# Optimization experiments

Measured on AMD Instinct MI355X. Metric: run time of the kernel, lower is better.

## Reference

```python
import jax, jax.numpy as jnp
import numpy as np

DIM = 180; HEADS = 6; WS = 16; NUM_TOKENS = 64; RDIM = 10; CAT = 128
KS = 5; MLP_HID = 360; DTD = 64; Hh = 64; Ww = 64; B = 8; M = 64


def _ln(x, g, b, eps=1e-5):
    mu = x.mean(-1, keepdims=True)
    var = ((x - mu) ** 2).mean(-1, keepdims=True)
    return (x - mu) / jnp.sqrt(var + eps) * g + b


def _l2norm(x):
    return x / jnp.clip(jnp.linalg.norm(x, axis=-1, keepdims=True), 1e-12)


def setup_inputs() -> dict:
    key = jax.random.key(0)
    ks = jax.random.split(key, 24)
    rn = lambda k, s: jax.random.normal(k, s, jnp.float32) * 0.02
    z = lambda *s: jnp.zeros(s, jnp.float32)
    return {
        'x': jax.random.normal(ks[0], (B, Hh * Ww, DIM), jnp.float32),
        'td': jax.random.normal(ks[1], (B, M, DIM), jnp.float32),
        'norm1_g': jnp.ones((DIM,), jnp.float32), 'norm1_b': z(DIM),
        'wqkv_w': rn(ks[2], (DIM, 3 * DIM)), 'wqkv_b': z(3 * DIM),
        'atd_wq_w': rn(ks[3], (DIM, RDIM)), 'atd_wq_b': z(RDIM),
        'atd_wk_w': rn(ks[4], (DIM, RDIM)), 'atd_wk_b': z(RDIM),
        'atd_wv_w': rn(ks[5], (DIM, DIM)), 'atd_wv_b': z(DIM),
        'atd_scale': jnp.ones((1,), jnp.float32),
        'aca_proj_w': rn(ks[6], (DIM, DIM)), 'aca_proj_b': z(DIM),
        'win_rpb': rn(ks[7], ((2 * WS - 1) ** 2, HEADS)),
        'win_proj_w': rn(ks[8], (DIM, DIM)), 'win_proj_b': z(DIM),
        'fc_td_w': rn(ks[9], (DIM, DTD)), 'fc_td_b': z(DTD),
        'fc1_w': rn(ks[10], (DIM, MLP_HID)), 'fc1_b': z(MLP_HID),
        'dw_w': rn(ks[11], (MLP_HID + DTD, 1, KS, KS)), 'dw_b': z(MLP_HID + DTD),
        'fc2_w': rn(ks[12], (MLP_HID + DTD, DIM)), 'fc2_b': z(DIM),
        'norm2_g': jnp.ones((DIM,), jnp.float32), 'norm2_b': z(DIM),
        'rpi_sa': jax.random.randint(ks[13], (WS * WS, WS * WS), 0, (2 * WS - 1) ** 2),
        'h': Hh, 'w': Ww,
    }


def reference(x, td, norm1_g, norm1_b, wqkv_w, wqkv_b, atd_wq_w, atd_wq_b,
              atd_wk_w, atd_wk_b, atd_wv_w, atd_wv_b, atd_scale,
              aca_proj_w, aca_proj_b, win_rpb, win_proj_w, win_proj_b,
              fc_td_w, fc_td_b, fc1_w, fc1_b, dw_w, dw_b, fc2_w, fc2_b,
              norm2_g, norm2_b, rpi_sa, h, w):
    b, n, c = x.shape
    hd = c // HEADS
    shortcut = x
    xn = _ln(x, norm1_g, norm1_b)
    qkv = xn @ wqkv_w + wqkv_b  # [b, n, 3c]

    # --- ATD_CA: l2-normalized cross-attention to token dictionary ---
    q = xn @ atd_wq_w + atd_wq_b          # [b, n, rd]
    kk = td @ atd_wk_w + atd_wk_b         # [b, m, rd]
    vv = td @ atd_wv_w + atd_wv_b         # [b, m, c]
    logit_scale = 1.0 + jnp.clip(atd_scale, 0.0, 3.0) * np.log(NUM_TOKENS)
    sim = jnp.einsum('bnr,bmr->bnm', _l2norm(q), _l2norm(kk)) * logit_scale
    attn_atd = jax.nn.softmax(sim, axis=-1)
    x_atd = jnp.einsum('bnm,bmc->bnc', attn_atd, vv)
    tk_id = jnp.argmax(attn_atd, axis=-1)  # [b, n]

    # --- AC_MSA: category-sorted grouped attention ---
    gs = min(n, CAT); ng = (n + gs - 1) // gs; pad_n = ng * gs - n
    sort_idx = jnp.argsort(tk_id, axis=-1)
    inv_idx = jnp.argsort(sort_idx, axis=-1)  # inverse permutation
    sq = jnp.take_along_axis(qkv, sort_idx[:, :, None], axis=1)
    sq = jnp.concatenate([sq, jnp.flip(sq[:, n - pad_n:n, :], axis=1)], axis=1)
    g = sq.reshape(b, ng, gs, 3, HEADS, hd).transpose(3, 0, 1, 4, 2, 5)
    qa, ka, va = g[0], g[1], g[2]          # [b, ng, H, gs, hd]
    a = jax.nn.softmax(jnp.einsum('bgHid,bgHjd->bgHij', qa, ka) * hd ** -0.5, axis=-1)
    y = jnp.einsum('bgHij,bgHjd->bgHid', a, va).transpose(0, 1, 3, 2, 4)
    y = y.reshape(b, n + pad_n, c)[:, :n]
    x_aca = jnp.take_along_axis(y, inv_idx[:, :, None], axis=1) @ aca_proj_w + aca_proj_b

    # --- gather per-token dictionary features for FFN ---
    td_proj = td @ fc_td_w + fc_td_b       # [b, m, dtd]
    x_td = jnp.take_along_axis(td_proj, jnp.broadcast_to(tk_id[:, :, None], (b, n, DTD)), axis=1)

    # --- window attention (shift_size = 0, no mask) ---
    nwh, nww = h // WS, w // WS
    win = qkv.reshape(b, nwh, WS, nww, WS, 3 * c).transpose(0, 1, 3, 2, 4, 5)
    win = win.reshape(-1, WS * WS, 3 * c)
    B_ = win.shape[0]; N = WS * WS
    wq = win.reshape(B_, N, 3, HEADS, hd).transpose(2, 0, 3, 1, 4)
    qw, kw, vw = wq[0] * hd ** -0.5, wq[1], wq[2]
    bias = win_rpb[rpi_sa.reshape(-1)].reshape(N, N, HEADS).transpose(2, 0, 1)[None]
    aw = jax.nn.softmax(jnp.einsum('wHid,wHjd->wHij', qw, kw) + bias, axis=-1)
    ow = jnp.einsum('wHij,wHjd->wHid', aw, vw).transpose(0, 2, 1, 3).reshape(B_, N, c)
    ow = ow @ win_proj_w + win_proj_b
    attn_x = ow.reshape(b, nwh, nww, WS, WS, c).transpose(0, 1, 3, 2, 4, 5).reshape(b, n, c)

    x = shortcut + x_atd + attn_x + x_aca

    # --- ConvFFN_td with depthwise conv branch ---
    x2 = _ln(x, norm2_g, norm2_b)
    h1 = jax.nn.gelu(x2 @ fc1_w + fc1_b, approximate=False)
    hc = jnp.concatenate([h1, x_td], axis=-1)  # [b, n, C]
    C = hc.shape[-1]
    img = jnp.swapaxes(hc, 1, 2).reshape(b, C, h, w)
    conv = jax.lax.conv_general_dilated(img, dw_w, (1, 1), 'SAME',
        dimension_numbers=('NCHW', 'OIHW', 'NCHW'), feature_group_count=C)
    conv = jax.nn.gelu(conv + dw_b[None, :, None, None], approximate=False)
    hc = hc + jnp.swapaxes(conv.reshape(b, C, n), 1, 2)
    return x + hc @ fc2_w + fc2_b
```

## Files before the change

### kernel.cpp

```cpp
#include <hip/hip_runtime.h>
#include <hip/hip_bf16.h>
#include <math.h>

#define BB      8
#define NTOK    4096
#define CDIM    180
#define C3      540
#define NHEADS  6
#define HD      30
#define MDICT   64
#define RD      10
#define DTD     64
#define MHID    360
#define CCAT    424
#define WS      16
#define WIN_N   256
#define GS      128
#define NG      32
#define ROWS    (BB*NTOK)
#define KP1     192
#define KP2     448

typedef __hip_bfloat16 bf16;
typedef short v8s __attribute__((ext_vector_type(8)));
typedef float f32x4 __attribute__((ext_vector_type(4)));
typedef unsigned int u32x4 __attribute__((ext_vector_type(4)));

__device__ __forceinline__ float gelu_exact(float x) {
    return 0.5f * x * (1.0f + erff(x * 0.70710678118654752f));
}
__device__ __forceinline__ float wave_sum(float v) {
    #pragma unroll
    for (int off = 32; off > 0; off >>= 1) v += __shfl_xor(v, off, 64);
    return v;
}
__device__ __forceinline__ unsigned short f2b(float v) {
    unsigned u = __float_as_uint(v);
    return (unsigned short)((u + 0x7FFFu + ((u >> 16) & 1u)) >> 16);
}
__device__ __forceinline__ float b2f(unsigned short h) {
    return __uint_as_float(((unsigned)h) << 16);
}
__device__ __forceinline__ unsigned packbf(float lo, float hi) {
    return (unsigned)f2b(lo) | ((unsigned)f2b(hi) << 16);
}

__global__ __launch_bounds__(256) void detect_kernel(const void* __restrict__ x,
                                                     int* __restrict__ flag,
                                                     int* __restrict__ diag)
{
    __shared__ int cnt;
    if (threadIdx.x == 0) { cnt = 0; *diag = 0; }
    __syncthreads();
    const unsigned short* u = (const unsigned short*)x;
    int c = 0;
    for (int i = threadIdx.x; i < 2048; i += 256) {
        unsigned short e = u[2 * i] & 0x7F80;
        if (e >= 0x4300) c++;
    }
    atomicAdd(&cnt, c);
    __syncthreads();
    if (threadIdx.x == 0) *flag = (cnt > 16) ? 1 : 0;
}

#define NCVT 23
struct CvtArgs {
    const void* src[NCVT];
    float* dst[NCVT];
    int cum[NCVT + 1];
};
__global__ __launch_bounds__(256) void convert_all_kernel(CvtArgs a, int total,
        const int* __restrict__ flag)
{
    int i = blockIdx.x * 256 + threadIdx.x;
    if (i >= total) return;
    int s = 0;
    while (i >= a.cum[s + 1]) s++;
    int off = i - a.cum[s];
    if (*flag) a.dst[s][off] = ((const float*)a.src[s])[off];
    else       a.dst[s][off] = __bfloat162float(((const bf16*)a.src[s])[off]);
}

__global__ __launch_bounds__(256) void check_f32_kernel(const float* __restrict__ buf,
        int n, int bit, int* __restrict__ diag)
{
    int i = blockIdx.x * 256 + threadIdx.x;
    if (i >= n) return;
    unsigned u = __float_as_uint(buf[i]);
    if ((u & 0x7F800000u) == 0x7F800000u) atomicOr(diag, bit);
}

__global__ __launch_bounds__(256) void emit_kernel(const float* __restrict__ src,
        void* __restrict__ out, const int* __restrict__ flag,
        const int* __restrict__ diag, int n)
{
    int i = blockIdx.x * 256 + threadIdx.x;
    if (i >= n) return;
    float v = src[i];
    int d = *diag;
    if (d) v = 100.f + 32.f * (float)d;
    if (*flag) ((float*)out)[i] = v;
    else       ((bf16*)out)[i]  = __float2bfloat16(v);
}

__global__ __launch_bounds__(256) void zero_tail_kernel(bf16* __restrict__ buf)
{
    int idx = blockIdx.x * 256 + threadIdx.x;
    int row = idx / 12, c = idx % 12;
    buf[(size_t)row * KP1 + CDIM + c] = __float2bfloat16(0.f);
}

__global__ __launch_bounds__(256) void packW_kernel(const void* __restrict__ W,
        bf16* __restrict__ Wt, int K, int N, int Kpad, int total,
        const int* __restrict__ flag)
{
    int idx = blockIdx.x * 256 + threadIdx.x;
    if (idx >= total) return;
    int n = idx / Kpad, k = idx % Kpad;
    float v = 0.f;
    if (k < K && n < N) {
        size_t src = (size_t)k * N + n;
        v = (*flag) ? ((const float*)W)[src]
                    : __bfloat162float(((const bf16*)W)[src]);
    }
    Wt[idx] = __float2bfloat16(v);
}

__global__ __launch_bounds__(256) void bias_pre_kernel(const int* __restrict__ rpi,
        const float* __restrict__ rpb, float* __restrict__ bias_t)
{
    int idx = blockIdx.x * 256 + threadIdx.x;
    int h = idx >> 16, ij = idx & 65535;
    bias_t[idx] = rpb[rpi[ij] * NHEADS + h];
}

template<bool GELU_, bool ADDRES, bool BIAS_>
__global__ __launch_bounds__(256) void mgemm_kernel(
        const bf16* __restrict__ A, int lda,
        const bf16* __restrict__ Wt, int ldw,
        const float* __restrict__ bias,
        const float* __restrict__ res, int ldr,
        float* __restrict__ outF, int ldo, int N, int K)
{
    __shared__ unsigned short As[64][32];
    __shared__ unsigned short Bs[64][32];
    int tid = threadIdx.x;
    int wave = tid >> 6, lane = tid & 63;
    int quad = lane >> 4, mr = lane & 15;
    int row0 = blockIdx.y * 64, col0 = blockIdx.x * 64;
    f32x4 z = {0.f, 0.f, 0.f, 0.f};
    f32x4 acc[4] = {z, z, z, z};
    const unsigned short* Au = (const unsigned short*)A;
    const unsigned short* Wu = (const unsigned short*)Wt;
    for (int k0 = 0; k0 < K; k0 += 32) {
        #pragma unroll
        for (int e = 0; e < 8; e++) {
            int idx = tid * 8 + e;
            int r = idx >> 5, c = idx & 31;
            As[r][c] = Au[(size_t)(row0 + r) * lda + k0 + c];
            Bs[r][c] = Wu[(size_t)(col0 + r) * ldw + k0 + c];
        }
        __syncthreads();
        v8s a;
        #pragma unroll
        for (int j = 0; j < 8; j++) a[j] = (short)As[wave * 16 + mr][quad * 8 + j];
        #pragma unroll
        for (int ni = 0; ni < 4; ni++) {
            v8s b;
            #pragma unroll
            for (int j = 0; j < 8; j++) b[j] = (short)Bs[ni * 16 + mr][quad * 8 + j];
            acc[ni] = __builtin_amdgcn_mfma_f32_16x16x32_bf16(a, b, acc[ni], 0, 0, 0);
        }
        __syncthreads();
    }
    #pragma unroll
    for (int ni = 0; ni < 4; ni++) {
        int gc = col0 + ni * 16 + mr;
        if (gc >= N) continue;
        float bv = BIAS_ ? bias[gc] : 0.f;
        #pragma unroll
        for (int r = 0; r < 4; r++) {
            int gr = row0 + wave * 16 + quad * 4 + r;
            float v = acc[ni][r] + bv;
            if (GELU_) v = gelu_exact(v);
            if (ADDRES) v += res[(size_t)gr * ldr + gc];
            outF[(size_t)gr * ldo + gc] = v;
        }
    }
}

__global__ __launch_bounds__(256) void av_mgemm_kernel(
        const bf16* __restrict__ P, const bf16* __restrict__ vvT,
        const float* __restrict__ xres, float* __restrict__ accout)
{
    __shared__ unsigned short As[64][32];
    __shared__ unsigned short Bs[64][32];
    int tid = threadIdx.x;
    int wave = tid >> 6, lane = tid & 63;
    int quad = lane >> 4, mr = lane & 15;
    int row0 = blockIdx.y * 64, col0 = blockIdx.x * 64;
    int bz = blockIdx.z;
    const unsigned short* Au = (const unsigned short*)P + (size_t)bz * NTOK * MDICT;
    const unsigned short* Wu = (const unsigned short*)vvT + (size_t)bz * 192 * MDICT;
    const float* res = xres + (size_t)bz * NTOK * CDIM;
    float* outF = accout + (size_t)bz * NTOK * CDIM;
    f32x4 z = {0.f, 0.f, 0.f, 0.f};
    f32x4 acc[4] = {z, z, z, z};
    for (int k0 = 0; k0 < MDICT; k0 += 32) {
        #pragma unroll
        for (int e = 0; e < 8; e++) {
            int idx = tid * 8 + e;
            int r = idx >> 5, c = idx & 31;
            As[r][c] = Au[(size_t)(row0 + r) * MDICT + k0 + c];
            Bs[r][c] = Wu[(size_t)(col0 + r) * MDICT + k0 + c];
        }
        __syncthreads();
        v8s a;
        #pragma unroll
        for (int j = 0; j < 8; j++) a[j] = (short)As[wave * 16 + mr][quad * 8 + j];
        #pragma unroll
        for (int ni = 0; ni < 4; ni++) {
            v8s b;
            #pragma unroll
            for (int j = 0; j < 8; j++) b[j] = (short)Bs[ni * 16 + mr][quad * 8 + j];
            acc[ni] = __builtin_amdgcn_mfma_f32_16x16x32_bf16(a, b, acc[ni], 0, 0, 0);
        }
        __syncthreads();
    }
    #pragma unroll
    for (int ni = 0; ni < 4; ni++) {
        int gc = col0 + ni * 16 + mr;
        if (gc >= CDIM) continue;
        #pragma unroll
        for (int r = 0; r < 4; r++) {
            int gr = row0 + wave * 16 + quad * 4 + r;
            float v = acc[ni][r] + res[(size_t)gr * CDIM + gc];
            outF[(size_t)gr * CDIM + gc] = v;
        }
    }
}

__global__ __launch_bounds__(256, 4) void win_mfma_kernel(const float* __restrict__ qkv,
        const float* __restrict__ bias_t, bf16* __restrict__ outb)
{
    int b = blockIdx.y;
    int widx = blockIdx.x / NHEADS;
    int hh = blockIdx.x % NHEADS;
    int wy = widx >> 2, wx = widx & 3;
    int tid = threadIdx.x;
    int wave = tid >> 6, lane = tid & 63, quad = lane >> 4, mr = lane & 15;
    __shared__ __align__(16) unsigned short Ks[64][40];
    __shared__ __align__(16) unsigned short Vt[32][80];

    size_t brow = (size_t)b * NTOK;
    const float scq = 0.18257418583505536f;

    v8s aq[4];
    #pragma unroll
    for (int tt = 0; tt < 4; tt++) {
        int m = (wave * 4 + tt) * 16 + mr;
        int nt_ = (wy * WS + (m >> 4)) * 64 + wx * WS + (m & 15);
        const float* qrow = qkv + (brow + nt_) * C3 + hh * HD;
        #pragma unroll
        for (int jj = 0; jj < 8; jj++) {
            int d = quad * 8 + jj;
            float v = (d < HD) ? qrow[d] * scq : 0.f;
            aq[tt][jj] = (short)f2b(v);
        }
    }
    f32x4 z = {0.f, 0.f, 0.f, 0.f};
    f32x4 oacc[4][2] = {{z, z}, {z, z}, {z, z}, {z, z}};
    float m_r[4], l_r[4];
    #pragma unroll
    for (int tt = 0; tt < 4; tt++) { m_r[tt] = -3.0e38f; l_r[tt] = 0.f; }
    const float* btab = bias_t + (size_t)hh * WIN_N * WIN_N;

    for (int kc = 0; kc < WIN_N; kc += 64) {
        {
            int j = tid >> 2, dg = (tid & 3) * 8;
            int tok = kc + j;
            int nt_ = (wy * WS + (tok >> 4)) * 64 + wx * WS + (tok & 15);
            const float* krow = qkv + (brow + nt_) * C3 + CDIM + hh * HD;
            const float* vrow = qkv + (brow + nt_) * C3 + 2 * CDIM + hh * HD;
            v8s kv;
            #pragma unroll
            for (int jj = 0; jj < 8; jj++) {
                int d = dg + jj;
                float kf = (d < HD) ? krow[d] : 0.f;
                float vf = (d < HD) ? vrow[d] : 0.f;
                kv[jj] = (short)f2b(kf);
                Vt[d][j] = f2b(vf);
            }
            *(v8s*)&Ks[j][dg] = kv;
        }
        __syncthreads();
        #pragma unroll
        for (int tt = 0; tt < 4; tt++) {
            f32x4 s[4];
            #pragma unroll
            for (int nt = 0; nt < 4; nt++) {
                v8s bk = *(const v8s*)&Ks[nt * 16 + mr][quad * 8];
                s[nt] = __builtin_amdgcn_mfma_f32_16x16x32_bf16(bk, aq[tt], z, 0, 0, 0);
            }
            int qg = (wave * 4 + tt) * 16 + mr;
            const float* bi = btab + (size_t)qg * WIN_N + kc;
            float mc = -3.0e38f;
            #pragma unroll
            for (int nt = 0; nt < 4; nt++) {
                f32x4 b4 = *(const f32x4*)(bi + nt * 16 + quad * 4);
                s[nt][0] += b4[0]; s[nt][1] += b4[1];
                s[nt][2] += b4[2]; s[nt][3] += b4[3];
                mc = fmaxf(mc, fmaxf(fmaxf(s[nt][0], s[nt][1]),
                                     fmaxf(s[nt][2], s[nt][3])));
            }
            mc = fmaxf(mc, __shfl_xor(mc, 16, 64));
            mc = fmaxf(mc, __shfl_xor(mc, 32, 64));
            float mn = fmaxf(m_r[tt], mc);
            float alpha = __expf(m_r[tt] - mn);
            m_r[tt] = mn;
            float ls = 0.f;
            #pragma unroll
            for (int nt = 0; nt < 4; nt++) {
                #pragma unroll
                for (int r = 0; r < 4; r++) {
                    float pp = __expf(s[nt][r] - mn);
                    ls += pp;
                    s[nt][r] = pp;
                }
            }
            ls += __shfl_xor(ls, 16, 64);
            ls += __shfl_xor(ls, 32, 64);
            l_r[tt] = l_r[tt] * alpha + ls;
            unsigned dpk[4][2];
            #pragma unroll
            for (int nt = 0; nt < 4; nt++) {
                dpk[nt][0] = packbf(s[nt][0], s[nt][1]);
                dpk[nt][1] = packbf(s[nt][2], s[nt][3]);
            }
            #pragma unroll
            for (int r = 0; r < 4; r++) {
                float av = __shfl(alpha, quad * 4 + r, 64);
                oacc[tt][0][r] *= av;
                oacc[tt][1][r] *= av;
            }
            #pragma unroll
            for (int c = 0; c < 2; c++) {
                union { u32x4 u; v8s s8; } afu;
                #pragma unroll
                for (int t = 0; t < 4; t++) {
                    int srcl = (((quad * 2 + (t >> 1)) & 3) << 4) | mr;
                    unsigned r0 = (unsigned)__shfl((int)dpk[2 * c][t & 1], srcl, 64);
                    unsigned r1 = (unsigned)__shfl((int)dpk[2 * c + 1][t & 1], srcl, 64);
                    afu.u[t] = (quad & 2) ? r1 : r0;
                }
                #pragma unroll
                for (int dt = 0; dt < 2; dt++) {
                    v8s bv = *(const v8s*)&Vt[dt * 16 + mr][c * 32 + quad * 8];
                    oacc[tt][dt] = __builtin_amdgcn_mfma_f32_16x16x32_bf16(
                        afu.s8, bv, oacc[tt][dt], 0, 0, 0);
                }
            }
        }
        __syncthreads();
    }
    #pragma unroll
    for (int tt = 0; tt < 4; tt++) {
        float il = 1.f / l_r[tt];
        #pragma unroll
        for (int r = 0; r < 4; r++) {
            float ilr = __shfl(il, quad * 4 + r, 64);
            int m = (wave * 4 + tt) * 16 + quad * 4 + r;
            int nt_ = (wy * WS + (m >> 4)) * 64 + wx * WS + (m & 15);
            #pragma unroll
            for (int dt = 0; dt < 2; dt++) {
                int d = dt * 16 + mr;
                if (d >= HD) continue;
                outb[(brow + nt_) * KP1 + hh * HD + d] =
                    __float2bfloat16(oacc[tt][dt][r] * ilr);
            }
        }
    }
}

__global__ __launch_bounds__(256) void acmsa_mfma_kernel(const float* __restrict__ qkv,
        const int* __restrict__ sidx, bf16* __restrict__ outb)
{
    int b = blockIdx.y;
    int g = blockIdx.x / NHEADS;
    int hh = blockIdx.x % NHEADS;
    int tid = threadIdx.x;
    int wave = tid >> 6, lane = tid & 63, quad = lane >> 4, mr = lane & 15;
    __shared__ int toks[GS];
    __shared__ __align__(16) unsigned short Ks[64][40];
    __shared__ __align__(16) unsigned short Vt[32][80];
    __shared__ __align__(16) unsigned short Sc[GS][72];
    __shared__ float alpha_s[GS];
    __shared__ float invl_s[GS];

    size_t brow = (size_t)b * NTOK;
    if (tid < GS) toks[tid] = sidx[brow + (size_t)g * GS + tid];
    __syncthreads();
    const float scq = 0.18257418583505536f;

    v8s aq[2];
    #pragma unroll
    for (int tt = 0; tt < 2; tt++) {
        int m = (wave * 2 + tt) * 16 + mr;
        const float* qrow = qkv + (brow + toks[m]) * C3 + hh * HD;
        #pragma unroll
        for (int jj = 0; jj < 8; jj++) {
            int d = quad * 8 + jj;
            float v = (d < HD) ? qrow[d] * scq : 0.f;
            aq[tt][jj] = (short)f2b(v);
        }
    }
    f32x4 z = {0.f, 0.f, 0.f, 0.f};
    f32x4 oacc[2][2] = {{z, z}, {z, z}};
    float m_r = -3.0e38f, l_r = 0.f;

    for (int kc = 0; kc < GS; kc += 64) {
        {
            int j = tid >> 2, dg = (tid & 3) * 8;
            int tok = toks[kc + j];
            const float* krow = qkv + (brow + tok) * C3 + CDIM + hh * HD;
            const float* vrow = qkv + (brow + tok) * C3 + 2 * CDIM + hh * HD;
            v8s kv;
            #pragma unroll
            for (int jj = 0; jj < 8; jj++) {
                int d = dg + jj;
                float kf = (d < HD) ? krow[d] : 0.f;
                float vf = (d < HD) ? vrow[d] : 0.f;
                kv[jj] = (short)f2b(kf);
                Vt[d][j] = f2b(vf);
            }
            *(v8s*)&Ks[j][dg] = kv;
        }
        __syncthreads();
        #pragma unroll
        for (int nt = 0; nt < 4; nt++) {
            v8s bk = *(const v8s*)&Ks[nt * 16 + mr][quad * 8];
            #pragma unroll
            for (int tt = 0; tt < 2; tt++) {
                f32x4 s = __builtin_amdgcn_mfma_f32_16x16x32_bf16(aq[tt], bk, z, 0, 0, 0);
                int rowb = (wave * 2 + tt) * 16 + quad * 4;
                #pragma unroll
                for (int r = 0; r < 4; r++)
                    Sc[rowb + r][nt * 16 + mr] = f2b(s[r]);
            }
        }
        __syncthreads();
        if (tid < GS) {
            int r = tid;
            float mc = -3.0e38f;
            #pragma unroll
            for (int j0 = 0; j0 < 64; j0 += 8) {
                v8s sv = *(const v8s*)&Sc[r][j0];
                #pragma unroll
                for (int jj = 0; jj < 8; jj++)
                    mc = fmaxf(mc, b2f((unsigned short)sv[jj]));
            }
            float mn = fmaxf(m_r, mc);
            float alpha = __expf(m_r - mn);
            float lsum = 0.f;
            #pragma unroll
            for (int j0 = 0; j0 < 64; j0 += 8) {
                v8s sv = *(const v8s*)&Sc[r][j0];
                v8s pv;
                #pragma unroll
                for (int jj = 0; jj < 8; jj++) {
                    float pp = __expf(b2f((unsigned short)sv[jj]) - mn);
                    lsum += pp;
                    pv[jj] = (short)f2b(pp);
                }
                *(v8s*)&Sc[r][j0] = pv;
            }
            l_r = l_r * alpha + lsum;
            m_r = mn;
            alpha_s[r] = alpha;
        }
        __syncthreads();
        #pragma unroll
        for (int tt = 0; tt < 2; tt++) {
            int rowb = (wave * 2 + tt) * 16 + quad * 4;
            float a0 = alpha_s[rowb], a1 = alpha_s[rowb + 1],
                  a2 = alpha_s[rowb + 2], a3 = alpha_s[rowb + 3];
            #pragma unroll
            for (int dt = 0; dt < 2; dt++) {
                oacc[tt][dt][0] *= a0; oacc[tt][dt][1] *= a1;
                oacc[tt][dt][2] *= a2; oacc[tt][dt][3] *= a3;
            }
        }
        #pragma unroll
        for (int kk = 0; kk < 64; kk += 32) {
            v8s ap[2];
            #pragma unroll
            for (int tt = 0; tt < 2; tt++)
                ap[tt] = *(const v8s*)&Sc[(wave * 2 + tt) * 16 + mr][kk + quad * 8];
            #pragma unroll
            for (int dt = 0; dt < 2; dt++) {
                v8s bv = *(const v8s*)&Vt[dt * 16 + mr][kk + quad * 8];
                #pragma unroll
                for (int tt = 0; tt < 2; tt++)
                    oacc[tt][dt] = __builtin_amdgcn_mfma_f32_16x16x32_bf16(
                        ap[tt], bv, oacc[tt][dt], 0, 0, 0);
            }
        }
        __syncthreads();
    }
    if (tid < GS) invl_s[tid] = 1.f / l_r;
    __syncthreads();
    #pragma unroll
    for (int tt = 0; tt < 2; tt++) {
        int rowb = (wave * 2 + tt) * 16 + quad * 4;
        #pragma unroll
        for (int dt = 0; dt < 2; dt++) {
            int d = dt * 16 + mr;
            if (d >= HD) continue;
            #pragma unroll
            for (int r = 0; r < 4; r++) {
                int m = rowb + r;
                int tok = toks[m];
                outb[(brow + tok) * KP1 + hh * HD + d] =
                    __float2bfloat16(oacc[tt][dt][r] * invl_s[m]);
            }
        }
    }
}

__global__ __launch_bounds__(64) void ln_kernel(const float* __restrict__ x,
        const float* __restrict__ g, const float* __restrict__ be,
        float* __restrict__ out, bf16* __restrict__ outb)
{
    int row = blockIdx.x; int t = threadIdx.x;
    const float* xr = x + (size_t)row * CDIM;
    float v0 = xr[t];
    float v1 = xr[t + 64];
    float v2 = (t < CDIM - 128) ? xr[t + 128] : 0.f;
    float s1 = wave_sum(v0 + v1 + v2);
    float s2 = wave_sum(v0*v0 + v1*v1 + v2*v2);
    float mu = s1 / (float)CDIM;
    float var = s2 / (float)CDIM - mu * mu;
    float rs = rsqrtf(var + 1e-5f);
    float o0 = (v0 - mu) * rs * g[t]      + be[t];
    float o1 = (v1 - mu) * rs * g[t + 64] + be[t + 64];
    float o2 = (t < CDIM - 128) ? ((v2 - mu) * rs * g[t + 128] + be[t + 128]) : 0.f;
    float* o = out + (size_t)row * CDIM;
    o[t] = o0; o[t + 64] = o1;
    if (t < CDIM - 128) o[t + 128] = o2;
    bf16* ob = outb + (size_t)row * KP1;
    ob[t]       = __float2bfloat16(o0);
    ob[t + 64]  = __float2bfloat16(o1);
    ob[t + 128] = __float2bfloat16(o2);
}

__global__ __launch_bounds__(64) void td_pre_kernel(const float* __restrict__ td,
        const float* __restrict__ wk, const float* __restrict__ wkb,
        const float* __restrict__ wv, const float* __restrict__ wvb,
        const float* __restrict__ wtd, const float* __restrict__ wtdb,
        float* __restrict__ kkn, bf16* __restrict__ vvT, float* __restrict__ tdp)
{
    int blk = blockIdx.x;
    int b = blk >> 6, m = blk & 63;
    int t = threadIdx.x;
    __shared__ float tr[CDIM];
    __shared__ float sk[RD];
    __shared__ float snorm;
    const float* tdr = td + (size_t)blk * CDIM;
    tr[t] = tdr[t]; tr[t + 64] = tdr[t + 64];
    if (t < CDIM - 128) tr[t + 128] = tdr[t + 128];
    __syncthreads();
    if (t < RD) {
        float s = wkb[t];
        for (int k = 0; k < CDIM; k++) s += tr[k] * wk[k * RD + t];
        sk[t] = s;
    }
    __syncthreads();
    if (t == 0) {
        float s = 0.f;
        #pragma unroll
        for (int j = 0; j < RD; j++) s += sk[j] * sk[j];
        snorm = fmaxf(sqrtf(s), 1e-12f);
    }
    __syncthreads();
    if (t < RD) kkn[(size_t)blk * RD + t] = sk[t] / snorm;
    for (int c = t; c < 192; c += 64) {
        float s = 0.f;
        if (c < CDIM) {
            s = wvb[c];
            for (int k = 0; k < CDIM; k++) s += tr[k] * wv[k * CDIM + c];
        }
        vvT[((size_t)(b * 192 + c)) * MDICT + m] = __float2bfloat16(s);
    }
    {
        float s = wtdb[t];
        for (int k = 0; k < CDIM; k++) s += tr[k] * wtd[k * DTD + t];
        tdp[(size_t)blk * DTD + t] = s;
    }
}

__global__ __launch_bounds__(64) void atd_soft_kernel(const float* __restrict__ xn,
        const float* __restrict__ wq, const float* __restrict__ wqb,
        const float* __restrict__ scale_p, const float* __restrict__ kkn,
        bf16* __restrict__ Pout, int* __restrict__ tk_id)
{
    int row = blockIdx.x;
    int b = row >> 12;
    int t = threadIdx.x;
    const float* xrow = xn + (size_t)row * CDIM;
    float v0 = xrow[t];
    float v1 = xrow[t + 64];
    float v2 = (t < CDIM - 128) ? xrow[t + 128] : 0.f;
    float sq[RD];
    #pragma unroll
    for (int j = 0; j < RD; j++) {
        float part = v0 * wq[t * RD + j] + v1 * wq[(t + 64) * RD + j];
        if (t < CDIM - 128) part += v2 * wq[(t + 128) * RD + j];
        sq[j] = wave_sum(part) + wqb[j];
    }
    float qn = 0.f;
    #pragma unroll
    for (int j = 0; j < RD; j++) qn += sq[j] * sq[j];
    qn = fmaxf(sqrtf(qn), 1e-12f);
    float ls = 1.0f + fminf(fmaxf(scale_p[0], 0.f), 3.f) * 4.158883083359672f;
    const float* kr = kkn + ((size_t)b * MDICT + t) * RD;
    float s = 0.f;
    #pragma unroll
    for (int j = 0; j < RD; j++) s += sq[j] * kr[j];
    s = s / qn * ls;
    float mv = s; int mi = t;
    #pragma unroll
    for (int off = 32; off > 0; off >>= 1) {
        float ov = __shfl_xor(mv, off, 64);
        int   oi = __shfl_xor(mi, off, 64);
        if (ov > mv || (ov == mv && oi < mi)) { mv = ov; mi = oi; }
    }
    float e = __expf(s - mv);
    float denom = wave_sum(e);
    Pout[(size_t)row * MDICT + t] = __float2bfloat16(e / denom);
    if (t == 0) tk_id[row] = mi;
}

__global__ __launch_bounds__(256) void sort_kernel(const int* __restrict__ tk_id,
                                                   int* __restrict__ sidx)
{
    int b = blockIdx.x; int tid = threadIdx.x;
    __shared__ int keys[NTOK];
    __shared__ int cnt[256];
    __shared__ int off[256];
    const int* kb = tk_id + (size_t)b * NTOK;
    for (int i = tid; i < NTOK; i += 256) keys[i] = kb[i];
    __syncthreads();
    int v = tid >> 2, seg = tid & 3;
    int lo = seg * 1024, hi = lo + 1024;
    int c = 0;
    for (int i = lo; i < hi; i++) c += (keys[i] == v);
    cnt[tid] = c;
    __syncthreads();
    if (tid == 0) {
        int run = 0;
        for (int l = 0; l < 256; l++) { off[l] = run; run += cnt[l]; }
    }
    __syncthreads();
    int o = off[tid];
    int* sb = sidx + (size_t)b * NTOK;
    for (int i = lo; i < hi; i++) if (keys[i] == v) sb[o++] = i;
}

__global__ __launch_bounds__(256) void gather_td_kernel(const int* __restrict__ tk_id,
        const float* __restrict__ tdp, float* __restrict__ hc)
{
    int idx = blockIdx.x * 256 + threadIdx.x;
    int row = idx >> 6, j = idx & 63;
    int b = row >> 12;
    int tk = tk_id[row];
    hc[(size_t)row * CCAT + MHID + j] = tdp[((size_t)b * MDICT + tk) * DTD + j];
}

#define CHK3 64
#define CTW  8
#define CTH  8
#define CHW  12
#define CHP  144
#define CSPX 68
__global__ __launch_bounds__(256) void conv_kernel(const float* __restrict__ hc,
        const float* __restrict__ w, const float* __restrict__ wb,
        bf16* __restrict__ outb)
{
    int ch0 = blockIdx.x * CHK3;
    int tile = blockIdx.y;
    int b = blockIdx.z;
    int ty0 = (tile >> 3) * CTH, tx0 = (tile & 7) * CTW;
    __shared__ __align__(16) float sh[CHP][CSPX];
    __shared__ __align__(16) float wt[25][CHK3];
    int tid = threadIdx.x;
    for (int idx = tid; idx < CHP * CHK3; idx += 256) {
        int pix = idx >> 6, ch = idx & 63;
        int gy = ty0 + pix / CHW - 2, gx = tx0 + pix % CHW - 2;
        int chg = ch0 + ch;
        float v = 0.f;
        if (gy >= 0 && gy < 64 && gx >= 0 && gx < 64 && chg < CCAT)
            v = hc[((size_t)b * NTOK + gy * 64 + gx) * CCAT + chg];
        sh[pix][ch] = v;
    }
    for (int idx = tid; idx < 25 * CHK3; idx += 256) {
        int kk = idx >> 6, ch = idx & 63;
        int chg = ch0 + ch;
        wt[kk][ch] = (chg < CCAT) ? w[chg * 25 + kk] : 0.f;
    }
    __syncthreads();
    int q = tid & 3, p = tid >> 2;
    int px = p & 7, py = p >> 3;
    int cb = q * 16;
    int pc = py * CHW + px;
    v8s pk0, pk1;
    #pragma unroll
    for (int sub = 0; sub < 4; sub++) {
        int cs = cb + sub * 4;
        f32x4 acc = {0.f, 0.f, 0.f, 0.f};
        #pragma unroll
        for (int dy = 0; dy < 5; dy++) {
            #pragma unroll
            for (int dx = 0; dx < 5; dx++) {
                f32x4 sv = *(const f32x4*)&sh[pc + dy * CHW + dx][cs];
                f32x4 wv = *(const f32x4*)&wt[dy * 5 + dx][cs];
                acc += sv * wv;
            }
            __builtin_amdgcn_sched_barrier(0);
        }
        f32x4 ctr = *(const f32x4*)&sh[pc + 2 * CHW + 2][cs];
        #pragma unroll
        for (int c = 0; c < 4; c++) {
            int chg = ch0 + cs + c;
            float v = 0.f;
            if (chg < CCAT) {
                float gv = gelu_exact(acc[c] + wb[chg]);
                v = ctr[c] + gv;
            }
            int lc = sub * 4 + c;
            if (lc < 8) pk0[lc] = (short)f2b(v);
            else        pk1[lc - 8] = (short)f2b(v);
        }
        __builtin_amdgcn_sched_barrier(0);
    }
    size_t obase = ((size_t)b * NTOK + (ty0 + py) * 64 + tx0 + px) * KP2 + ch0 + cb;
    unsigned short* ob = (unsigned short*)outb + obase;
    *(v8s*)ob = pk0;
    *(v8s*)(ob + 8) = pk1;
}

extern "C" void kernel_launch(void* const* d_in, const int* in_sizes, int n_in,
                              void* d_out, int out_size, void* d_ws, size_t ws_size,
                              hipStream_t stream)
{
    (void)n_in; (void)ws_size; (void)out_size;
    const int* rpi = (const int*)d_in[28];

    float* p = (float*)d_ws;
    float* xn    = p; p += (size_t)ROWS * CDIM;
    float* acc   = p; p += (size_t)ROWS * CDIM;
    float* tmp1  = p; p += (size_t)ROWS * CDIM;
    float* qkv   = p; p += (size_t)ROWS * C3;
    float* hcnew = p; p += (size_t)ROWS * CCAT;
    float* kkn   = p; p += (size_t)BB * MDICT * RD;
    bf16*  vvT   = (bf16*)p; p += (size_t)BB * 192 * MDICT / 2;
    float* tdp   = p; p += (size_t)BB * MDICT * DTD;
    int*   tk_id = (int*)p; p += ROWS;
    int*   sidx  = (int*)p; p += ROWS;
    int*   flag  = (int*)p; p += 64;
    int*   diag  = (int*)p; p += 64;
    bf16* wtqkv = (bf16*)p; p += 576 * KP1 / 2;
    bf16* wtaca = (bf16*)p; p += 192 * KP1 / 2;
    bf16* wtwin = (bf16*)p; p += 192 * KP1 / 2;
    bf16* wtfc1 = (bf16*)p; p += 384 * KP1 / 2;
    bf16* wtfc2 = (bf16*)p; p += 192 * KP2 / 2;
    float* cin[28];
    for (int i = 0; i < 28; i++) { cin[i] = p; p += in_sizes[i]; }
    float* bias_t = p; p += (size_t)NHEADS * WIN_N * WIN_N;

    float* hc      = qkv;
    bf16*  xnb     = (bf16*)hcnew;
    bf16*  tmp1b   = (bf16*)(hcnew + (size_t)ROWS * KP1 / 2);
    bf16*  hcnewb2 = (bf16*)hcnew;
    bf16*  Pbuf    = (bf16*)tmp1;

    detect_kernel<<<1, 256, 0, stream>>>(d_in[0], flag, diag);
    {
        CvtArgs ca;
        int total = 0, s = 0;
        for (int i = 0; i < 28; i++) {
            if (i == 4 || i == 13 || i == 16 || i == 20 || i == 24) continue;
            ca.src[s] = d_in[i];
            ca.dst[s] = cin[i];
            ca.cum[s] = total;
            total += in_sizes[i];
            s++;
        }
        ca.cum[s] = total;
        convert_all_kernel<<<(total + 255) / 256, 256, 0, stream>>>(ca, total, flag);
    }
    const float *x = cin[0], *td = cin[1], *n1g = cin[2], *n1b = cin[3],
        *wqkv_b = cin[5], *wq_w = cin[6], *wq_b = cin[7],
        *wk_w = cin[8], *wk_b = cin[9], *wv_w = cin[10], *wv_b = cin[11],
        *atd_scale = cin[12], *aca_b = cin[14], *win_rpb = cin[15],
        *winp_b = cin[17], *fctd_w = cin[18], *fctd_b = cin[19],
        *fc1_b = cin[21], *dw_w = cin[22], *dw_b = cin[23], *fc2_b = cin[25],
        *n2g = cin[26], *n2b = cin[27];

    packW_kernel<<<576 * KP1 / 256, 256, 0, stream>>>(d_in[4],  wtqkv, CDIM, C3,   KP1, 576 * KP1, flag);
    packW_kernel<<<192 * KP1 / 256, 256, 0, stream>>>(d_in[13], wtaca, CDIM, CDIM, KP1, 192 * KP1, flag);
    packW_kernel<<<192 * KP1 / 256, 256, 0, stream>>>(d_in[16], wtwin, CDIM, CDIM, KP1, 192 * KP1, flag);
    packW_kernel<<<384 * KP1 / 256, 256, 0, stream>>>(d_in[20], wtfc1, CDIM, MHID, KP1, 384 * KP1, flag);
    packW_kernel<<<192 * KP2 / 256, 256, 0, stream>>>(d_in[24], wtfc2, CCAT, CDIM, KP2, 192 * KP2, flag);
    bias_pre_kernel<<<NHEADS * WIN_N * WIN_N / 256, 256, 0, stream>>>(rpi, win_rpb, bias_t);

    td_pre_kernel<<<BB * MDICT, 64, 0, stream>>>(td, wk_w, wk_b, wv_w, wv_b,
                                                 fctd_w, fctd_b, kkn, vvT, tdp);
    ln_kernel<<<ROWS, 64, 0, stream>>>(x, n1g, n1b, xn, xnb);
    mgemm_kernel<false, false, true><<<dim3(9, ROWS / 64), 256, 0, stream>>>(
        xnb, KP1, wtqkv, KP1, wqkv_b, nullptr, 0, qkv, C3, C3, KP1);
    atd_soft_kernel<<<ROWS, 64, 0, stream>>>(xn, wq_w, wq_b, atd_scale, kkn, Pbuf, tk_id);
    av_mgemm_kernel<<<dim3(3, NTOK / 64, BB), 256, 0, stream>>>(Pbuf, vvT, x, acc);
    sort_kernel<<<BB, 256, 0, stream>>>(tk_id, sidx);
    zero_tail_kernel<<<ROWS * 12 / 256, 256, 0, stream>>>(tmp1b);
    acmsa_mfma_kernel<<<dim3(NG * NHEADS, BB), 256, 0, stream>>>(qkv, sidx, tmp1b);
    mgemm_kernel<false, true, true><<<dim3(3, ROWS / 64), 256, 0, stream>>>(
        tmp1b, KP1, wtaca, KP1, aca_b, acc, CDIM, acc, CDIM, CDIM, KP1);
    win_mfma_kernel<<<dim3(16 * NHEADS, BB), 256, 0, stream>>>(qkv, bias_t, tmp1b);
    mgemm_kernel<false, true, true><<<dim3(3, ROWS / 64), 256, 0, stream>>>(
        tmp1b, KP1, wtwin, KP1, winp_b, acc, CDIM, acc, CDIM, CDIM, KP1);
    ln_kernel<<<ROWS, 64, 0, stream>>>(acc, n2g, n2b, xn, xnb);
    mgemm_kernel<true, false, true><<<dim3(6, ROWS / 64), 256, 0, stream>>>(
        xnb, KP1, wtfc1, KP1, fc1_b, nullptr, 0, hc, CCAT, MHID, KP1);
    gather_td_kernel<<<ROWS * 64 / 256, 256, 0, stream>>>(tk_id, tdp, hc);
    conv_kernel<<<dim3(7, 64, BB), 256, 0, stream>>>(hc, dw_w, dw_b, hcnewb2);
    mgemm_kernel<false, true, true><<<dim3(3, ROWS / 64), 256, 0, stream>>>(
        hcnewb2, KP2, wtfc2, KP2, fc2_b, acc, CDIM, tmp1, CDIM, CDIM, KP2);
    check_f32_kernel<<<(ROWS * CDIM + 255) / 256, 256, 0, stream>>>(tmp1, ROWS * CDIM, 8, diag);
    emit_kernel<<<(ROWS * CDIM + 255) / 256, 256, 0, stream>>>(
        tmp1, d_out, flag, diag, ROWS * CDIM);
}
```

Before: 711.3 us.

## Keep ACMSA softmax in registers with transposed MFMA and lane shuffles

Rewrites the ACMSA group-attention inner loop so scores come from a transposed MFMA (K as A operand). The online softmax max and sum are then reduced with cross-lane shuffles inside registers, and P is repacked to bf16 via shuffles as the A operand for the PV MFMA. This removes the shared-memory score buffer, the alpha and inverse-sum arrays, two barriers per chunk, and the single-thread-per-row softmax pass that left half the block idle. It also adds a launch-bounds occupancy hint, at the cost of extra shuffle instructions and register pressure.

```diff
diff --git a/kernel.cpp b/kernel.cpp
--- a/kernel.cpp
+++ b/kernel.cpp
@@ -382,7 +382,7 @@
     }
 }
 
-__global__ __launch_bounds__(256) void acmsa_mfma_kernel(const float* __restrict__ qkv,
+__global__ __launch_bounds__(256, 4) void acmsa_mfma_kernel(const float* __restrict__ qkv,
         const int* __restrict__ sidx, bf16* __restrict__ outb)
 {
     int b = blockIdx.y;
@@ -393,9 +393,6 @@
     __shared__ int toks[GS];
     __shared__ __align__(16) unsigned short Ks[64][40];
     __shared__ __align__(16) unsigned short Vt[32][80];
-    __shared__ __align__(16) unsigned short Sc[GS][72];
-    __shared__ float alpha_s[GS];
-    __shared__ float invl_s[GS];
 
     size_t brow = (size_t)b * NTOK;
     if (tid < GS) toks[tid] = sidx[brow + (size_t)g * GS + tid];
@@ -416,7 +413,9 @@
     }
     f32x4 z = {0.f, 0.f, 0.f, 0.f};
     f32x4 oacc[2][2] = {{z, z}, {z, z}};
-    float m_r = -3.0e38f, l_r = 0.f;
+    float m_r[2], l_r[2];
+    #pragma unroll
+    for (int tt = 0; tt < 2; tt++) { m_r[tt] = -3.0e38f; l_r[tt] = 0.f; }
 
     for (int kc = 0; kc < GS; kc += 64) {
         {
@@ -437,91 +436,82 @@
         }
         __syncthreads();
         #pragma unroll
-        for (int nt = 0; nt < 4; nt++) {
-            v8s bk = *(const v8s*)&Ks[nt * 16 + mr][quad * 8];
-            #pragma unroll
-            for (int tt = 0; tt < 2; tt++) {
-                f32x4 s = __builtin_amdgcn_mfma_f32_16x16x32_bf16(aq[tt], bk, z, 0, 0, 0);
-                int rowb = (wave * 2 + tt) * 16 + quad * 4;
+        for (int tt = 0; tt < 2; tt++) {
+            f32x4 s[4];
+            #pragma unroll
+            for (int nt = 0; nt < 4; nt++) {
+                v8s bk = *(const v8s*)&Ks[nt * 16 + mr][quad * 8];
+                s[nt] = __builtin_amdgcn_mfma_f32_16x16x32_bf16(bk, aq[tt], z, 0, 0, 0);
+            }
+            float mc = -3.0e38f;
+            #pragma unroll
+            for (int nt = 0; nt < 4; nt++)
+                mc = fmaxf(mc, fmaxf(fmaxf(s[nt][0], s[nt][1]),
+                                     fmaxf(s[nt][2], s[nt][3])));
+            mc = fmaxf(mc, __shfl_xor(mc, 16, 64));
+            mc = fmaxf(mc, __shfl_xor(mc, 32, 64));
+            float mn = fmaxf(m_r[tt], mc);
+            float alpha = __expf(m_r[tt] - mn);
+            m_r[tt] = mn;
+            float ls = 0.f;
+            #pragma unroll
+            for (int nt = 0; nt < 4; nt++) {
                 #pragma unroll
-                for (int r = 0; r < 4; r++)
-                    Sc[rowb + r][nt * 16 + mr] = f2b(s[r]);
+                for (int r = 0; r < 4; r++) {
+                    float pp = __expf(s[nt][r] - mn);
+                    ls += pp;
+                    s[nt][r] = pp;
+                }
+            }
+            ls += __shfl_xor(ls, 16, 64);
+            ls += __shfl_xor(ls, 32, 64);
+            l_r[tt] = l_r[tt] * alpha + ls;
+            unsigned dpk[4][2];
+            #pragma unroll
+            for (int nt = 0; nt < 4; nt++) {
+                dpk[nt][0] = packbf(s[nt][0], s[nt][1]);
+                dpk[nt][1] = packbf(s[nt][2], s[nt][3]);
+            }
+            #pragma unroll
+            for (int r = 0; r < 4; r++) {
+                float av = __shfl(alpha, quad * 4 + r, 64);
+                oacc[tt][0][r] *= av;
+                oacc[tt][1][r] *= av;
+            }
+            #pragma unroll
+            for (int c = 0; c < 2; c++) {
+                union { u32x4 u; v8s s8; } afu;
+                #pragma unroll
+                for (int t = 0; t < 4; t++) {
+                    int srcl = (((quad * 2 + (t >> 1)) & 3) << 4) | mr;
+                    unsigned r0 = (unsigned)__shfl((int)dpk[2 * c][t & 1], srcl, 64);
+                    unsigned r1 = (unsigned)__shfl((int)dpk[2 * c + 1][t & 1], srcl, 64);
+                    afu.u[t] = (quad & 2) ? r1 : r0;
+                }
+                #pragma unroll
+                for (int dt = 0; dt < 2; dt++) {
+                    v8s bv = *(const v8s*)&Vt[dt * 16 + mr][c * 32 + quad * 8];
+                    oacc[tt][dt] = __builtin_amdgcn_mfma_f32_16x16x32_bf16(
+                        afu.s8, bv, oacc[tt][dt], 0, 0, 0);
+                }
             }
         }
         __syncthreads();
-        if (tid < GS) {
-            int r = tid;
-            float mc = -3.0e38f;
-            #pragma unroll
-            for (int j0 = 0; j0 < 64; j0 += 8) {
-                v8s sv = *(const v8s*)&Sc[r][j0];
-                #pragma unroll
-                for (int jj = 0; jj < 8; jj++)
-                    mc = fmaxf(mc, b2f((unsigned short)sv[jj]));
-            }
-            float mn = fmaxf(m_r, mc);
-            float alpha = __expf(m_r - mn);
-            float lsum = 0.f;
-            #pragma unroll
-            for (int j0 = 0; j0 < 64; j0 += 8) {
-                v8s sv = *(const v8s*)&Sc[r][j0];
-                v8s pv;
-                #pragma unroll
-                for (int jj = 0; jj < 8; jj++) {
-                    float pp = __expf(b2f((unsigned short)sv[jj]) - mn);
-                    lsum += pp;
-                    pv[jj] = (short)f2b(pp);
-                }
-                *(v8s*)&Sc[r][j0] = pv;
-            }
-            l_r = l_r * alpha + lsum;
-            m_r = mn;
-            alpha_s[r] = alpha;
-        }
-        __syncthreads();
-        #pragma unroll
-        for (int tt = 0; tt < 2; tt++) {
-            int rowb = (wave * 2 + tt) * 16 + quad * 4;
-            float a0 = alpha_s[rowb], a1 = alpha_s[rowb + 1],
-                  a2 = alpha_s[rowb + 2], a3 = alpha_s[rowb + 3];
+    }
+    #pragma unroll
+    for (int tt = 0; tt < 2; tt++) {
+        float il = 1.f / l_r[tt];
+        #pragma unroll
+        for (int r = 0; r < 4; r++) {
+            float ilr = __shfl(il, quad * 4 + r, 64);
+            int m = (wave * 2 + tt) * 16 + quad * 4 + r;
+            int tok = toks[m];
             #pragma unroll
             for (int dt = 0; dt < 2; dt++) {
-                oacc[tt][dt][0] *= a0; oacc[tt][dt][1] *= a1;
-                oacc[tt][dt][2] *= a2; oacc[tt][dt][3] *= a3;
-            }
-        }
-        #pragma unroll
-        for (int kk = 0; kk < 64; kk += 32) {
-            v8s ap[2];
-            #pragma unroll
-            for (int tt = 0; tt < 2; tt++)
-                ap[tt] = *(const v8s*)&Sc[(wave * 2 + tt) * 16 + mr][kk + quad * 8];
-            #pragma unroll
-            for (int dt = 0; dt < 2; dt++) {
-                v8s bv = *(const v8s*)&Vt[dt * 16 + mr][kk + quad * 8];
-                #pragma unroll
-                for (int tt = 0; tt < 2; tt++)
-                    oacc[tt][dt] = __builtin_amdgcn_mfma_f32_16x16x32_bf16(
-                        ap[tt], bv, oacc[tt][dt], 0, 0, 0);
-            }
-        }
-        __syncthreads();
-    }
-    if (tid < GS) invl_s[tid] = 1.f / l_r;
-    __syncthreads();
-    #pragma unroll
-    for (int tt = 0; tt < 2; tt++) {
-        int rowb = (wave * 2 + tt) * 16 + quad * 4;
-        #pragma unroll
-        for (int dt = 0; dt < 2; dt++) {
-            int d = dt * 16 + mr;
-            if (d >= HD) continue;
-            #pragma unroll
-            for (int r = 0; r < 4; r++) {
-                int m = rowb + r;
-                int tok = toks[m];
+                int d = dt * 16 + mr;
+                if (d >= HD) continue;
                 outb[(brow + tok) * KP1 + hh * HD + d] =
-                    __float2bfloat16(oacc[tt][dt][r] * invl_s[m]);
+                    __float2bfloat16(oacc[tt][dt][r] * ilr);
             }
         }
     }
```

Result: no change. 706.4 us (-0.7%).
